# Performance work log

Measured on AMD Instinct MI355X. Metric: run time of the kernel, lower is better.

The kernel has to match this reference:

```python
import jax, jax.numpy as jnp
import numpy as np

SPATIAL = 128   # spatial_grid (H == W)
CROP = 256      # temporal grid T (power of 2)
BIN_LEN = 0.01
WALL_SIZE = 2.0
SNR = 0.1
DNUM = 2        # feature channels; bnum fixed to 1 by the module


def definePsf(U, V, slope):
    # Matlab-faithful LCT light-cone PSF: shape (2V, 2U, 2U) = (2T, 2H, 2W)
    x = np.linspace(-1.0, 1.0, 2 * U)
    z = np.linspace(0.0, 2.0, 2 * V)
    grid_z, grid_y, grid_x = np.meshgrid(z, x, x, indexing='ij')
    psf = np.abs((4.0 * slope) ** 2 * (grid_x ** 2 + grid_y ** 2) - grid_z)
    psf = (psf == psf.min(axis=0, keepdims=True)).astype(np.float64)
    psf = psf / psf[:, U, U].sum()
    psf = psf / np.linalg.norm(psf.ravel())
    psf = np.roll(psf, U, axis=1)
    psf = np.roll(psf, U, axis=2)
    return psf


def resamplingOperator(M):
    # mtx: MxM resampling (t -> sqrt-time), mtxi: its transpose-downsampled inverse
    mtx = np.zeros((M * M, M), dtype=np.float64)
    x = np.arange(1, M * M + 1)
    mtx[x - 1, np.ceil(np.sqrt(x)).astype(np.int64) - 1] = 1.0
    mtx = mtx / np.sqrt(x)[:, None]
    mtxi = mtx.T.copy()
    for _ in range(int(round(np.log2(M)))):
        mtx = 0.5 * (mtx[0::2, :] + mtx[1::2, :])
        mtxi = 0.5 * (mtxi[:, 0::2] + mtxi[:, 1::2])
    return mtx.astype(np.float32), mtxi.astype(np.float32)


def setup_inputs() -> dict:
    key = jax.random.key(0)
    c = 3e8
    bin_resolution = BIN_LEN / c
    trange = CROP * c * bin_resolution
    slope = (WALL_SIZE / 2.0) / trange
    psf = definePsf(SPATIAL, CROP, slope)
    fpsf = np.fft.fftn(psf)
    # Wiener-style inverse filter ('lct' method)
    invpsf = np.conjugate(fpsf) / (1.0 / SNR + np.real(fpsf) ** 2 + np.imag(fpsf) ** 2)
    mtx, mtxi = resamplingOperator(CROP)
    gridz = (np.arange(CROP, dtype=np.float32) / (CROP - 1)).reshape(1, CROP, 1, 1)
    feature = jax.random.normal(key, (1, DNUM, CROP, SPATIAL, SPATIAL), dtype=jnp.float32)
    return {
        'feature': feature,
        'gridz': jnp.asarray(gridz),                      # [1, T, 1, 1]
        'mtx': jnp.asarray(mtx),                          # [T, T]
        'mtxi': jnp.asarray(mtxi),                        # [T, T]
        'invpsf_real': jnp.asarray(np.real(invpsf).astype(np.float32))[None],  # [1, 2T, 2H, 2W]
        'invpsf_imag': jnp.asarray(np.imag(invpsf).astype(np.float32))[None],
    }


def reference(feature, gridz, mtx, mtxi, invpsf_real, invpsf_imag):
    b, d, T, H, W = feature.shape
    # radiometric falloff correction (diffuse: z^4)
    data = feature.reshape(b * d, T, H, W) * gridz ** 4
    # temporal resampling matmul: [T,T] @ [BD, T, H*W]
    tmp = jnp.einsum('mt,bthw->bmhw', mtx, data)
    # zero-pad to (2T, 2H, 2W)
    pad = jnp.zeros((b * d, 2 * T, 2 * H, 2 * W), dtype=feature.dtype)
    pad = pad.at[:, :T, :H, :W].set(tmp)
    # full complex 3D FFT (original stacks real/imag and calls torch.fft(x, 3))
    fre = jnp.fft.fftn(pad, axes=(1, 2, 3))
    invpsf = jax.lax.complex(invpsf_real, invpsf_imag)
    vol = jnp.fft.ifftn(fre * invpsf, axes=(1, 2, 3)).real[:, :T, :H, :W]
    out = jnp.einsum('mt,bthw->bmhw', mtxi, vol)
    return out.reshape(b, d, T, H, W)
```

## Files before the change

### kernel.cpp

```cpp
#include <hip/hip_runtime.h>
#include <math.h>

typedef float2 cplx;
#define PI_F 3.14159265358979323846f
#define C8F 0.70710678118654752440f

__device__ __forceinline__ cplx cadd(cplx a, cplx b){ return make_float2(a.x+b.x, a.y+b.y); }
__device__ __forceinline__ cplx csub(cplx a, cplx b){ return make_float2(a.x-b.x, a.y-b.y); }
__device__ __forceinline__ cplx cmul(cplx a, cplx b){ return make_float2(a.x*b.x - a.y*b.y, a.x*b.y + a.y*b.x); }
__device__ __forceinline__ cplx cmulc(cplx a, cplx b){ return make_float2(a.x*b.x + a.y*b.y, a.y*b.x - a.x*b.y); }
__device__ __forceinline__ cplx cax(float s, cplx v){ return make_float2(s*v.x, s*v.y); }

template<bool INV>
__device__ __forceinline__ void dft8(cplx* v) {
    cplx t0 = cadd(v[0], v[4]), u0 = csub(v[0], v[4]);
    cplx t1 = cadd(v[1], v[5]), u1 = csub(v[1], v[5]);
    cplx t2 = cadd(v[2], v[6]), u2 = csub(v[2], v[6]);
    cplx t3 = cadd(v[3], v[7]), u3 = csub(v[3], v[7]);
    if (!INV) {
        u1 = make_float2(C8F*(u1.x + u1.y), C8F*(u1.y - u1.x));
        u2 = make_float2(u2.y, -u2.x);
        u3 = make_float2(C8F*(u3.y - u3.x), -C8F*(u3.x + u3.y));
    } else {
        u1 = make_float2(C8F*(u1.x - u1.y), C8F*(u1.x + u1.y));
        u2 = make_float2(-u2.y, u2.x);
        u3 = make_float2(-C8F*(u3.x + u3.y), C8F*(u3.x - u3.y));
    }
    cplx b0 = cadd(t0,t2), b1 = cadd(t1,t3), b2 = csub(t0,t2), b3 = csub(t1,t3);
    b3 = INV ? make_float2(-b3.y, b3.x) : make_float2(b3.y, -b3.x);
    v[0] = cadd(b0,b1); v[4] = csub(b0,b1); v[2] = cadd(b2,b3); v[6] = csub(b2,b3);
    cplx c0 = cadd(u0,u2), c1 = cadd(u1,u3), c2 = csub(u0,u2), c3 = csub(u1,u3);
    c3 = INV ? make_float2(-c3.y, c3.x) : make_float2(c3.y, -c3.x);
    v[1] = cadd(c0,c1); v[5] = csub(c0,c1); v[3] = cadd(c2,c3); v[7] = csub(c2,c3);
}

template<bool INV>
__device__ __forceinline__ void dft4(cplx* v) {
    cplx b0 = cadd(v[0], v[2]), b2 = csub(v[0], v[2]);
    cplx b1 = cadd(v[1], v[3]), b3 = csub(v[1], v[3]);
    b3 = INV ? make_float2(-b3.y, b3.x) : make_float2(b3.y, -b3.x);
    v[0] = cadd(b0,b1); v[2] = csub(b0,b1); v[1] = cadd(b2,b3); v[3] = csub(b2,b3);
}

template<bool INV>
__device__ __forceinline__ void dft16(cplx* v) {
    #pragma unroll
    for (int a = 0; a < 4; ++a) {
        cplx t[4] = { v[a], v[a+4], v[a+8], v[a+12] };
        dft4<INV>(t);
        v[a] = t[0]; v[a+4] = t[1]; v[a+8] = t[2]; v[a+12] = t[3];
    }
    const float C1 = 0.92387953251128674f, S1 = 0.38268343236508978f, R2 = 0.70710678118654752f;
    #define TWX(idx, CR, CI) v[idx] = cmul(v[idx], make_float2(CR, INV ? -(CI) : (CI)))
    TWX(1+4*1,  C1, -S1);
    TWX(1+4*2,  R2, -R2);
    TWX(1+4*3,  S1, -C1);
    TWX(2+4*1,  R2, -R2);
    TWX(2+4*2, 0.f, -1.f);
    TWX(2+4*3, -R2, -R2);
    TWX(3+4*1,  S1, -C1);
    TWX(3+4*2, -R2, -R2);
    TWX(3+4*3, -C1,  S1);
    #undef TWX
    cplx o[16];
    #pragma unroll
    for (int c = 0; c < 4; ++c) {
        cplx t[4] = { v[4*c+0], v[4*c+1], v[4*c+2], v[4*c+3] };
        dft4<INV>(t);
        o[c] = t[0]; o[c+4] = t[1]; o[c+8] = t[2]; o[c+12] = t[3];
    }
    #pragma unroll
    for (int i = 0; i < 16; ++i) v[i] = o[i];
}

__device__ __forceinline__ int twp(int i){ return i + (i >> 4); }

__host__ __device__ __forceinline__ size_t idxB(int t, int h, int w) {
    return ((size_t)t * 256 + h) * 128 + w;
}

__global__ __launch_bounds__(256) void k0_mtx(
        const float* __restrict__ mtx, const float* __restrict__ gridz,
        float* __restrict__ tv, int* __restrict__ tc) {
    int m = blockIdx.x, t = threadIdx.x;
    __shared__ float rv[256];
    float g = gridz[t]; float g2 = g * g;
    rv[t] = mtx[m * 256 + t] * (g2 * g2);
    __syncthreads();
    if (t == 0) {
        int cnt = 0;
        for (int k = 0; k < 256 && cnt < 16; ++k)
            if (rv[k] != 0.f) { tv[m*16 + cnt] = rv[k]; tc[m*16 + cnt] = k; ++cnt; }
        for (; cnt < 16; ++cnt) { tv[m*16 + cnt] = 0.f; tc[m*16 + cnt] = 0; }
    }
}

__global__ __launch_bounds__(256) void k0_mtxi(
        const float* __restrict__ mtxi, float* __restrict__ tv, int* __restrict__ tc) {
    int m = blockIdx.x, t = threadIdx.x;
    __shared__ float rv[256];
    rv[t] = mtxi[m * 256 + t];
    __syncthreads();
    if (t == 0) {
        int cnt = 0;
        for (int k = 0; k < 256 && cnt < 8; ++k)
            if (rv[k] != 0.f) { tv[m*8 + cnt] = rv[k]; tc[m*8 + cnt] = k; ++cnt; }
        for (; cnt < 8; ++cnt) { tv[m*8 + cnt] = 0.f; tc[m*8 + cnt] = 0; }
    }
}

__global__ __launch_bounds__(512, 2) void k2_fftt(
        const float* __restrict__ feat, const float* __restrict__ tv,
        const int* __restrict__ tc, cplx* __restrict__ B) {
    const int h = blockIdx.x, w0 = blockIdx.y * 16;
    const int tid = threadIdx.x, ww = tid & 15, q = tid >> 4;
    __shared__ cplx buf[512 * 17];
    __shared__ cplx tw[512];
    { float s, c; sincosf(-(2.0f*PI_F/512.0f)*(float)tid, &s, &c); tw[tid] = make_float2(c, s); }
    cplx* f2 = buf;
    for (int idx = tid; idx < 4096; idx += 512) {
        int t = idx >> 4, w = idx & 15;
        size_t o = ((size_t)t * 128 + h) * 128 + w0 + w;
        f2[idx] = make_float2(feat[o], feat[o + 4194304]);
    }
    __syncthreads();
    cplx xa[2][8];
    for (int hi = 0; hi < 2; ++hi) {
        int u = q + 32*hi;
        #pragma unroll
        for (int p = 0; p < 8; ++p) {
            if (p < 4) {
                int m = u + 64*p;
                cplx acc = make_float2(0.f, 0.f);
                const float4* v4 = (const float4*)(tv + m*16);
                const int4*  c4 = (const int4*)(tc + m*16);
                #pragma unroll
                for (int jj = 0; jj < 4; ++jj) {
                    float4 vv = v4[jj]; int4 cc = c4[jj];
                    acc = cadd(acc, cax(vv.x, f2[cc.x*16 + ww]));
                    acc = cadd(acc, cax(vv.y, f2[cc.y*16 + ww]));
                    acc = cadd(acc, cax(vv.z, f2[cc.z*16 + ww]));
                    acc = cadd(acc, cax(vv.w, f2[cc.w*16 + ww]));
                }
                xa[hi][p] = acc;
            } else xa[hi][p] = make_float2(0.f, 0.f);
        }
    }
    dft8<false>(xa[0]); dft8<false>(xa[1]);
    __syncthreads();
    for (int hi = 0; hi < 2; ++hi) {
        int u = q + 32*hi;
        #pragma unroll
        for (int r = 1; r < 8; ++r) xa[hi][r] = cmul(xa[hi][r], tw[u * r]);
        #pragma unroll
        for (int r = 0; r < 8; ++r) buf[(64*r + u) * 17 + ww] = xa[hi][r];
    }
    __syncthreads();
    for (int hi = 0; hi < 2; ++hi) {
        int u = q + 32*hi, r1 = u >> 3, j = u & 7, base = 64*r1 + j;
        cplx y[8];
        #pragma unroll
        for (int p = 0; p < 8; ++p) y[p] = buf[(base + 8*p) * 17 + ww];
        dft8<false>(y);
        #pragma unroll
        for (int r2 = 1; r2 < 8; ++r2) y[r2] = cmul(y[r2], tw[8 * j * r2]);
        #pragma unroll
        for (int r2 = 0; r2 < 8; ++r2) buf[(base + 8*r2) * 17 + ww] = y[r2];
    }
    __syncthreads();
    for (int hi = 0; hi < 2; ++hi) {
        int m = q + 32*hi;
        cplx z[8];
        #pragma unroll
        for (int r = 0; r < 8; ++r) z[r] = buf[(8*m + r) * 17 + ww];
        dft8<false>(z);
        int kb = (m >> 3) + 8 * (m & 7);
        #pragma unroll
        for (int s2 = 0; s2 < 8; ++s2)
            B[idxB(kb + 64*s2, h, w0 + ww)] = z[s2];
    }
}

__global__ __launch_bounds__(256) void k3_ffth(cplx* __restrict__ B) {
    const int t = blockIdx.x, w0 = blockIdx.y * 16;
    const int tid = threadIdx.x, ww = tid & 15, q = tid >> 4;
    __shared__ cplx buf[256 * 16];
    __shared__ cplx tw[272];
    { float s, c; sincosf(-(2.0f*PI_F/256.0f)*(float)tid, &s, &c); tw[twp(tid)] = make_float2(c, s); }
    cplx x[16];
    #pragma unroll
    for (int n2 = 0; n2 < 8; ++n2) x[n2] = B[idxB(t, q + 16*n2, w0 + ww)];
    #pragma unroll
    for (int n2 = 8; n2 < 16; ++n2) x[n2] = make_float2(0.f, 0.f);
    dft16<false>(x);
    __syncthreads();
    #pragma unroll
    for (int k2 = 1; k2 < 16; ++k2) x[k2] = cmul(x[k2], tw[twp(q * k2)]);
    #pragma unroll
    for (int k2 = 0; k2 < 16; ++k2) buf[(q + 16*k2) * 16 + ww] = x[k2];
    __syncthreads();
    cplx z[16];
    #pragma unroll
    for (int n1 = 0; n1 < 16; ++n1) z[n1] = buf[(n1 + 16*q) * 16 + ww];
    dft16<false>(z);
    #pragma unroll
    for (int k1 = 0; k1 < 16; ++k1) B[idxB(t, q + 16*k1, w0 + ww)] = z[k1];
}

__global__ __launch_bounds__(256) void k4_fftw(
        cplx* __restrict__ B, const float* __restrict__ pr, const float* __restrict__ pim) {
    const int kt = blockIdx.x, kh0 = blockIdx.y * 16;
    const int tid = threadIdx.x, q = tid & 15, l = tid >> 4;
    __shared__ cplx buf[16 * 256];
    __shared__ cplx tw[272];
    { float s, c; sincosf(-(2.0f*PI_F/256.0f)*(float)tid, &s, &c); tw[twp(tid)] = make_float2(c, s); }
    const size_t lineB = idxB(kt, kh0 + l, 0);
    const size_t lineP = ((size_t)kt * 256 + kh0 + l) * 256;
    cplx x[16];
    #pragma unroll
    for (int n2 = 0; n2 < 8; ++n2) x[n2] = B[lineB + q + 16*n2];
    #pragma unroll
    for (int n2 = 8; n2 < 16; ++n2) x[n2] = make_float2(0.f, 0.f);
    float prv[16], piv[16];
    #pragma unroll
    for (int k1 = 0; k1 < 16; ++k1) {
        prv[k1] = pr[lineP + q + 16*k1];
        piv[k1] = pim[lineP + q + 16*k1];
    }
    dft16<false>(x);
    __syncthreads();
    #pragma unroll
    for (int k2 = 1; k2 < 16; ++k2) x[k2] = cmul(x[k2], tw[twp(q * k2)]);
    #pragma unroll
    for (int k2 = 0; k2 < 16; ++k2) buf[l*256 + (q ^ k2) + 16*k2] = x[k2];
    __syncthreads();
    cplx z[16];
    #pragma unroll
    for (int n1 = 0; n1 < 16; ++n1) z[n1] = buf[l*256 + (n1 ^ q) + 16*q];
    dft16<false>(z);
    const float S = 1.0f / (512.0f * 256.0f * 256.0f);
    #pragma unroll
    for (int k1 = 0; k1 < 16; ++k1)
        z[k1] = cmul(z[k1], make_float2(prv[k1]*S, piv[k1]*S));
    dft16<true>(z);
    #pragma unroll
    for (int n1 = 1; n1 < 16; ++n1) z[n1] = cmulc(z[n1], tw[twp(n1 * q)]);
    #pragma unroll
    for (int n1 = 0; n1 < 16; ++n1) buf[l*256 + (n1 ^ q) + 16*q] = z[n1];
    __syncthreads();
    cplx y[16];
    #pragma unroll
    for (int k2 = 0; k2 < 16; ++k2) y[k2] = buf[l*256 + (q ^ k2) + 16*k2];
    dft16<true>(y);
    #pragma unroll
    for (int n2 = 0; n2 < 8; ++n2) B[lineB + q + 16*n2] = y[n2];
}

__global__ __launch_bounds__(256) void k5_iffth(cplx* __restrict__ B) {
    const int t = blockIdx.x, w0 = blockIdx.y * 16;
    const int tid = threadIdx.x, ww = tid & 15, q = tid >> 4;
    __shared__ cplx buf[256 * 16];
    __shared__ cplx tw[272];
    { float s, c; sincosf(-(2.0f*PI_F/256.0f)*(float)tid, &s, &c); tw[twp(tid)] = make_float2(c, s); }
    cplx x[16];
    #pragma unroll
    for (int k1 = 0; k1 < 16; ++k1) x[k1] = B[idxB(t, q + 16*k1, w0 + ww)];
    dft16<true>(x);
    __syncthreads();
    #pragma unroll
    for (int n1 = 1; n1 < 16; ++n1) x[n1] = cmulc(x[n1], tw[twp(n1 * q)]);
    #pragma unroll
    for (int n1 = 0; n1 < 16; ++n1) buf[(n1 + 16*q) * 16 + ww] = x[n1];
    __syncthreads();
    cplx z[16];
    #pragma unroll
    for (int k2 = 0; k2 < 16; ++k2) z[k2] = buf[(q + 16*k2) * 16 + ww];
    dft16<true>(z);
    #pragma unroll
    for (int n2 = 0; n2 < 8; ++n2) B[idxB(t, q + 16*n2, w0 + ww)] = z[n2];
}

__global__ __launch_bounds__(512, 2) void k6_ifftt(
        cplx* __restrict__ B, const float* __restrict__ tv, const int* __restrict__ tc,
        float* __restrict__ out) {
    const int h = blockIdx.x, w0 = blockIdx.y * 16;
    const int tid = threadIdx.x, ww = tid & 15, q = tid >> 4;
    __shared__ cplx buf[512 * 17];
    __shared__ cplx tw[512];
    { float s, c; sincosf(-(2.0f*PI_F/512.0f)*(float)tid, &s, &c); tw[tid] = make_float2(c, s); }
    cplx za[2][8];
    for (int hi = 0; hi < 2; ++hi) {
        int m = q + 32*hi, kb = (m >> 3) + 8 * (m & 7);
        #pragma unroll
        for (int s2 = 0; s2 < 8; ++s2) za[hi][s2] = B[idxB(kb + 64*s2, h, w0 + ww)];
    }
    for (int hi = 0; hi < 2; ++hi) {
        int m = q + 32*hi;
        dft8<true>(za[hi]);
        #pragma unroll
        for (int jj = 0; jj < 8; ++jj) buf[(8*m + jj) * 17 + ww] = za[hi][jj];
    }
    __syncthreads();
    for (int hi = 0; hi < 2; ++hi) {
        int u = q + 32*hi, r1 = u >> 3, j = u & 7, base = 64*r1 + j;
        cplx y[8];
        #pragma unroll
        for (int r2 = 0; r2 < 8; ++r2) y[r2] = buf[(base + 8*r2) * 17 + ww];
        #pragma unroll
        for (int r2 = 1; r2 < 8; ++r2) y[r2] = cmulc(y[r2], tw[8 * j * r2]);
        dft8<true>(y);
        #pragma unroll
        for (int p = 0; p < 8; ++p) buf[(base + 8*p) * 17 + ww] = y[p];
    }
    __syncthreads();
    cplx vol[2][4];
    for (int hi = 0; hi < 2; ++hi) {
        int u = q + 32*hi;
        cplx xo[8];
        #pragma unroll
        for (int r = 0; r < 8; ++r) xo[r] = buf[(64*r + u) * 17 + ww];
        #pragma unroll
        for (int r = 1; r < 8; ++r) xo[r] = cmulc(xo[r], tw[u * r]);
        dft8<true>(xo);
        #pragma unroll
        for (int p = 0; p < 4; ++p) vol[hi][p] = xo[p];
    }
    __syncthreads();
    for (int hi = 0; hi < 2; ++hi) {
        int u = q + 32*hi;
        #pragma unroll
        for (int p = 0; p < 4; ++p) buf[(u + 64*p) * 16 + ww] = vol[hi][p];
    }
    __syncthreads();
    for (int hi = 0; hi < 2; ++hi) {
        int u = q + 32*hi;
        #pragma unroll
        for (int p = 0; p < 4; ++p) {
            int m = u + 64*p;
            cplx acc = make_float2(0.f, 0.f);
            const float4* v4 = (const float4*)(tv + m*8);
            const int4*  c4 = (const int4*)(tc + m*8);
            #pragma unroll
            for (int jj = 0; jj < 2; ++jj) {
                float4 vv = v4[jj]; int4 cc = c4[jj];
                acc = cadd(acc, cax(vv.x, buf[cc.x*16 + ww]));
                acc = cadd(acc, cax(vv.y, buf[cc.y*16 + ww]));
                acc = cadd(acc, cax(vv.z, buf[cc.z*16 + ww]));
                acc = cadd(acc, cax(vv.w, buf[cc.w*16 + ww]));
            }
            out[((size_t)m * 128 + h) * 128 + w0 + ww] = acc.x;
            out[(((size_t)256 + m) * 128 + h) * 128 + w0 + ww] = acc.y;
        }
    }
}

extern "C" void kernel_launch(void* const* d_in, const int* in_sizes, int n_in,
                              void* d_out, int out_size, void* d_ws, size_t ws_size,
                              hipStream_t stream) {
    const float* feat  = (const float*)d_in[0];
    const float* gridz = (const float*)d_in[1];
    const float* mtx   = (const float*)d_in[2];
    const float* mtxi  = (const float*)d_in[3];
    const float* pr    = (const float*)d_in[4];
    const float* pim   = (const float*)d_in[5];
    cplx* B = (cplx*)d_ws;
    float* out = (float*)d_out;

    float* T1v = (float*)(B + idxB(257, 128, 0));
    int*   T1c = (int*)(T1v + 4096);
    float* T2v = (float*)(B + idxB(0, 128, 0));
    int*   T2c = (int*)(T2v + 2048);

    k0_mtx <<<256, 256, 0, stream>>>(mtx, gridz, T1v, T1c);
    k2_fftt<<<dim3(128, 8), 512, 0, stream>>>(feat, T1v, T1c, B);
    k3_ffth<<<dim3(512, 8), 256, 0, stream>>>(B);
    k4_fftw<<<dim3(512, 16), 256, 0, stream>>>(B, pr, pim);
    k5_iffth<<<dim3(512, 8), 256, 0, stream>>>(B);
    k0_mtxi<<<256, 256, 0, stream>>>(mtxi, T2v, T2c);
    k6_ifftt<<<dim3(128, 8), 512, 0, stream>>>(B, T2v, T2c, out);
}
```

Before: 497.9 us.

## Exploit Hermitian symmetry of inverse PSF to halve filter reads in fftw kernel

Each k4 block now processes a frequency line and its mirrored line (-kt,-kh). For the mirrored line it reuses the PSF values of the first line, reading them at reversed indices and conjugating. This halves global reads of the large real/imag filter arrays and halves the grid. The 1/N normalisation is moved from the k4 filter multiply into the mtxi coefficients. The approach relies on invpsf being Hermitian-symmetric, which holds because the PSF is real, but would be wrong for an arbitrary complex filter input.

```diff
diff --git a/kernel.cpp b/kernel.cpp
--- a/kernel.cpp
+++ b/kernel.cpp
@@ -98,13 +98,14 @@
 __global__ __launch_bounds__(256) void k0_mtxi(
         const float* __restrict__ mtxi, float* __restrict__ tv, int* __restrict__ tc) {
     int m = blockIdx.x, t = threadIdx.x;
+    const float S = 2.9802322387695312e-08f;
     __shared__ float rv[256];
     rv[t] = mtxi[m * 256 + t];
     __syncthreads();
     if (t == 0) {
         int cnt = 0;
         for (int k = 0; k < 256 && cnt < 8; ++k)
-            if (rv[k] != 0.f) { tv[m*8 + cnt] = rv[k]; tc[m*8 + cnt] = k; ++cnt; }
+            if (rv[k] != 0.f) { tv[m*8 + cnt] = rv[k] * S; tc[m*8 + cnt] = k; ++cnt; }
         for (; cnt < 8; ++cnt) { tv[m*8 + cnt] = 0.f; tc[m*8 + cnt] = 0; }
     }
 }
@@ -207,53 +208,77 @@
     for (int k1 = 0; k1 < 16; ++k1) B[idxB(t, q + 16*k1, w0 + ww)] = z[k1];
 }
 
-__global__ __launch_bounds__(256) void k4_fftw(
+template<bool REV>
+__device__ __forceinline__ void k4_pass(
+        cplx* __restrict__ B, const float* __restrict__ pr, const float* __restrict__ pim,
+        size_t lineB, size_t lineP, int q, int l, cplx* buf, const cplx* tw, const cplx* xin) {
+    cplx x[16];
+    #pragma unroll
+    for (int n2 = 0; n2 < 8; ++n2) x[n2] = xin[n2];
+    #pragma unroll
+    for (int n2 = 8; n2 < 16; ++n2) x[n2] = make_float2(0.f, 0.f);
+    float prv[16], piv[16];
+    #pragma unroll
+    for (int k1 = 0; k1 < 16; ++k1) {
+        int ip = REV ? ((256 - (q + 16*k1)) & 255) : (q + 16*k1);
+        prv[k1] = pr[lineP + ip];
+        piv[k1] = pim[lineP + ip];
+    }
+    dft16<false>(x);
+    #pragma unroll
+    for (int k2 = 1; k2 < 16; ++k2) x[k2] = cmul(x[k2], tw[twp(q * k2)]);
+    #pragma unroll
+    for (int k2 = 0; k2 < 16; ++k2) buf[l*256 + (q ^ k2) + 16*k2] = x[k2];
+    __syncthreads();
+    cplx z[16];
+    #pragma unroll
+    for (int n1 = 0; n1 < 16; ++n1) z[n1] = buf[l*256 + (n1 ^ q) + 16*q];
+    dft16<false>(z);
+    #pragma unroll
+    for (int k1 = 0; k1 < 16; ++k1) {
+        cplx p = make_float2(prv[k1], piv[k1]);
+        z[k1] = REV ? cmulc(z[k1], p) : cmul(z[k1], p);
+    }
+    dft16<true>(z);
+    #pragma unroll
+    for (int n1 = 1; n1 < 16; ++n1) z[n1] = cmulc(z[n1], tw[twp(n1 * q)]);
+    #pragma unroll
+    for (int n1 = 0; n1 < 16; ++n1) buf[l*256 + (n1 ^ q) + 16*q] = z[n1];
+    __syncthreads();
+    cplx y[16];
+    #pragma unroll
+    for (int k2 = 0; k2 < 16; ++k2) y[k2] = buf[l*256 + (q ^ k2) + 16*k2];
+    dft16<true>(y);
+    #pragma unroll
+    for (int n2 = 0; n2 < 8; ++n2) B[lineB + q + 16*n2] = y[n2];
+}
+
+__global__ __launch_bounds__(256, 4) void k4_fftw(
         cplx* __restrict__ B, const float* __restrict__ pr, const float* __restrict__ pim) {
-    const int kt = blockIdx.x, kh0 = blockIdx.y * 16;
+    const int bx = blockIdx.x, kh0 = blockIdx.y * 16;
     const int tid = threadIdx.x, q = tid & 15, l = tid >> 4;
     __shared__ cplx buf[16 * 256];
     __shared__ cplx tw[272];
     { float s, c; sincosf(-(2.0f*PI_F/256.0f)*(float)tid, &s, &c); tw[twp(tid)] = make_float2(c, s); }
-    const size_t lineB = idxB(kt, kh0 + l, 0);
-    const size_t lineP = ((size_t)kt * 256 + kh0 + l) * 256;
-    cplx x[16];
-    #pragma unroll
-    for (int n2 = 0; n2 < 8; ++n2) x[n2] = B[lineB + q + 16*n2];
-    #pragma unroll
-    for (int n2 = 8; n2 < 16; ++n2) x[n2] = make_float2(0.f, 0.f);
-    float prv[16], piv[16];
-    #pragma unroll
-    for (int k1 = 0; k1 < 16; ++k1) {
-        prv[k1] = pr[lineP + q + 16*k1];
-        piv[k1] = pim[lineP + q + 16*k1];
-    }
-    dft16<false>(x);
-    __syncthreads();
-    #pragma unroll
-    for (int k2 = 1; k2 < 16; ++k2) x[k2] = cmul(x[k2], tw[twp(q * k2)]);
-    #pragma unroll
-    for (int k2 = 0; k2 < 16; ++k2) buf[l*256 + (q ^ k2) + 16*k2] = x[k2];
-    __syncthreads();
-    cplx z[16];
-    #pragma unroll
-    for (int n1 = 0; n1 < 16; ++n1) z[n1] = buf[l*256 + (n1 ^ q) + 16*q];
-    dft16<false>(z);
-    const float S = 1.0f / (512.0f * 256.0f * 256.0f);
-    #pragma unroll
-    for (int k1 = 0; k1 < 16; ++k1)
-        z[k1] = cmul(z[k1], make_float2(prv[k1]*S, piv[k1]*S));
-    dft16<true>(z);
-    #pragma unroll
-    for (int n1 = 1; n1 < 16; ++n1) z[n1] = cmulc(z[n1], tw[twp(n1 * q)]);
-    #pragma unroll
-    for (int n1 = 0; n1 < 16; ++n1) buf[l*256 + (n1 ^ q) + 16*q] = z[n1];
-    __syncthreads();
-    cplx y[16];
-    #pragma unroll
-    for (int k2 = 0; k2 < 16; ++k2) y[k2] = buf[l*256 + (q ^ k2) + 16*k2];
-    dft16<true>(y);
-    #pragma unroll
-    for (int n2 = 0; n2 < 8; ++n2) B[lineB + q + 16*n2] = y[n2];
+    const bool last = (bx == 255);
+    const int ktA = last ? 0 : bx + 1;
+    const int khA = kh0 + l;
+    const int ktB = last ? 256 : 512 - ktA;
+    const int khB = last ? khA : ((256 - khA) & 255);
+    const size_t lineBA = idxB(ktA, khA, 0);
+    const size_t lineBB = idxB(ktB, khB, 0);
+    const size_t linePA = ((size_t)ktA * 256 + khA) * 256;
+    const size_t linePB = last ? (((size_t)256 * 256 + khA) * 256) : linePA;
+    cplx xA[8], xB[8];
+    #pragma unroll
+    for (int n2 = 0; n2 < 8; ++n2) xA[n2] = B[lineBA + q + 16*n2];
+    #pragma unroll
+    for (int n2 = 0; n2 < 8; ++n2) xB[n2] = B[lineBB + q + 16*n2];
+    __syncthreads();
+    k4_pass<false>(B, pr, pim, lineBA, linePA, q, l, buf, tw, xA);
+    __syncthreads();
+    if (last) k4_pass<false>(B, pr, pim, lineBB, linePB, q, l, buf, tw, xB);
+    else      k4_pass<true >(B, pr, pim, lineBB, linePB, q, l, buf, tw, xB);
 }
 
 __global__ __launch_bounds__(256) void k5_iffth(cplx* __restrict__ B) {
@@ -374,7 +399,7 @@
     k0_mtx <<<256, 256, 0, stream>>>(mtx, gridz, T1v, T1c);
     k2_fftt<<<dim3(128, 8), 512, 0, stream>>>(feat, T1v, T1c, B);
     k3_ffth<<<dim3(512, 8), 256, 0, stream>>>(B);
-    k4_fftw<<<dim3(512, 16), 256, 0, stream>>>(B, pr, pim);
+    k4_fftw<<<dim3(256, 16), 256, 0, stream>>>(B, pr, pim);
     k5_iffth<<<dim3(512, 8), 256, 0, stream>>>(B);
     k0_mtxi<<<256, 256, 0, stream>>>(mtxi, T2v, T2c);
     k6_ifftt<<<dim3(128, 8), 512, 0, stream>>>(B, T2v, T2c, out);
```

Result: slower. 760.8 us (+52.8%).

## Fuse H-FFT, W-FFT/filter and inverse H-FFT into one per-plane kernel

Applied to the files above, without the earlier changes.

Replaces the three separate H-axis FFT, W-axis FFT+filter+IFFT and H-axis IFFT kernels with a single kernel that processes one whole kt plane in shared memory, split into even and odd frequency halves. It pairs kt with its mirror plane and exploits Hermitian symmetry of the PSF to index the filter. The global 1/N scale moves into the mtxi weights, and the odd and even halves are combined on the final write. This removes two full round trips of the large complex workspace through global memory, but uses 1024-thread blocks with 128KB of shared memory, which limits occupancy.

```diff
diff --git a/kernel.cpp b/kernel.cpp
--- a/kernel.cpp
+++ b/kernel.cpp
@@ -98,13 +98,14 @@
 __global__ __launch_bounds__(256) void k0_mtxi(
         const float* __restrict__ mtxi, float* __restrict__ tv, int* __restrict__ tc) {
     int m = blockIdx.x, t = threadIdx.x;
+    const float S = 2.9802322387695312e-08f;
     __shared__ float rv[256];
     rv[t] = mtxi[m * 256 + t];
     __syncthreads();
     if (t == 0) {
         int cnt = 0;
         for (int k = 0; k < 256 && cnt < 8; ++k)
-            if (rv[k] != 0.f) { tv[m*8 + cnt] = rv[k]; tc[m*8 + cnt] = k; ++cnt; }
+            if (rv[k] != 0.f) { tv[m*8 + cnt] = rv[k] * S; tc[m*8 + cnt] = k; ++cnt; }
         for (; cnt < 8; ++cnt) { tv[m*8 + cnt] = 0.f; tc[m*8 + cnt] = 0; }
     }
 }
@@ -181,103 +182,158 @@
     }
 }
 
-__global__ __launch_bounds__(256) void k3_ffth(cplx* __restrict__ B) {
-    const int t = blockIdx.x, w0 = blockIdx.y * 16;
-    const int tid = threadIdx.x, ww = tid & 15, q = tid >> 4;
-    __shared__ cplx buf[256 * 16];
+__device__ __forceinline__ void k4row(
+        cplx* __restrict__ eb, const int kh, const bool mir, const int ktp,
+        const int q, cplx* __restrict__ ex, const cplx* __restrict__ tw,
+        const float* __restrict__ pr, const float* __restrict__ pim) {
+    const int khp = mir ? ((256 - kh) & 255) : kh;
+    const size_t lineP = ((size_t)ktp * 256 + khp) * 256;
+    float prv[16], piv[16];
+    #pragma unroll
+    for (int k1 = 0; k1 < 16; ++k1) {
+        int kw = q + 16*k1;
+        int ip = mir ? ((256 - kw) & 255) : kw;
+        prv[k1] = pr[lineP + ip];
+        piv[k1] = mir ? -pim[lineP + ip] : pim[lineP + ip];
+    }
+    cplx x[16];
+    #pragma unroll
+    for (int n = 0; n < 8; ++n) x[n] = eb[n];
+    #pragma unroll
+    for (int n = 8; n < 16; ++n) x[n] = make_float2(0.f, 0.f);
+    dft16<false>(x);
+    #pragma unroll
+    for (int k2 = 1; k2 < 16; ++k2) x[k2] = cmul(x[k2], tw[twp(q * k2)]);
+    #pragma unroll
+    for (int k2 = 0; k2 < 16; ++k2) ex[(q ^ k2) + 16*k2] = x[k2];
+    __syncthreads();
+    cplx z[16];
+    #pragma unroll
+    for (int n1 = 0; n1 < 16; ++n1) z[n1] = ex[(n1 ^ q) + 16*q];
+    dft16<false>(z);
+    #pragma unroll
+    for (int k1 = 0; k1 < 16; ++k1) z[k1] = cmul(z[k1], make_float2(prv[k1], piv[k1]));
+    dft16<true>(z);
+    #pragma unroll
+    for (int n1 = 1; n1 < 16; ++n1) z[n1] = cmulc(z[n1], tw[twp(n1 * q)]);
+    #pragma unroll
+    for (int n1 = 0; n1 < 16; ++n1) ex[(n1 ^ q) + 16*q] = z[n1];
+    __syncthreads();
+    cplx y[16];
+    #pragma unroll
+    for (int k2 = 0; k2 < 16; ++k2) y[k2] = ex[(q ^ k2) + 16*k2];
+    dft16<true>(y);
+    #pragma unroll
+    for (int n = 0; n < 8; ++n) eb[n] = y[n];
+}
+
+__global__ __launch_bounds__(1024) void k345(
+        cplx* __restrict__ B, const float* __restrict__ pr, const float* __restrict__ pim) {
+    const int bx = blockIdx.x;
+    const int i = bx >> 1;
+    const int kt = ((bx & 1) == 0) ? i : (i == 0 ? 256 : 512 - i);
+    const bool mir = (kt > 256);
+    const int ktp = mir ? 512 - kt : kt;
+    const int tid = threadIdx.x;
+    const int w = tid & 127, b = tid >> 7;
+    const int team = tid >> 4, q = tid & 15;
+    __shared__ cplx PL[16384];
     __shared__ cplx tw[272];
-    { float s, c; sincosf(-(2.0f*PI_F/256.0f)*(float)tid, &s, &c); tw[twp(tid)] = make_float2(c, s); }
-    cplx x[16];
-    #pragma unroll
-    for (int n2 = 0; n2 < 8; ++n2) x[n2] = B[idxB(t, q + 16*n2, w0 + ww)];
-    #pragma unroll
-    for (int n2 = 8; n2 < 16; ++n2) x[n2] = make_float2(0.f, 0.f);
-    dft16<false>(x);
-    __syncthreads();
-    #pragma unroll
-    for (int k2 = 1; k2 < 16; ++k2) x[k2] = cmul(x[k2], tw[twp(q * k2)]);
-    #pragma unroll
-    for (int k2 = 0; k2 < 16; ++k2) buf[(q + 16*k2) * 16 + ww] = x[k2];
-    __syncthreads();
-    cplx z[16];
-    #pragma unroll
-    for (int n1 = 0; n1 < 16; ++n1) z[n1] = buf[(n1 + 16*q) * 16 + ww];
-    dft16<false>(z);
-    #pragma unroll
-    for (int k1 = 0; k1 < 16; ++k1) B[idxB(t, q + 16*k1, w0 + ww)] = z[k1];
-}
-
-__global__ __launch_bounds__(256) void k4_fftw(
-        cplx* __restrict__ B, const float* __restrict__ pr, const float* __restrict__ pim) {
-    const int kt = blockIdx.x, kh0 = blockIdx.y * 16;
-    const int tid = threadIdx.x, q = tid & 15, l = tid >> 4;
-    __shared__ cplx buf[16 * 256];
-    __shared__ cplx tw[272];
-    { float s, c; sincosf(-(2.0f*PI_F/256.0f)*(float)tid, &s, &c); tw[twp(tid)] = make_float2(c, s); }
-    const size_t lineB = idxB(kt, kh0 + l, 0);
-    const size_t lineP = ((size_t)kt * 256 + kh0 + l) * 256;
-    cplx x[16];
-    #pragma unroll
-    for (int n2 = 0; n2 < 8; ++n2) x[n2] = B[lineB + q + 16*n2];
-    #pragma unroll
-    for (int n2 = 8; n2 < 16; ++n2) x[n2] = make_float2(0.f, 0.f);
-    float prv[16], piv[16];
-    #pragma unroll
-    for (int k1 = 0; k1 < 16; ++k1) {
-        prv[k1] = pr[lineP + q + 16*k1];
-        piv[k1] = pim[lineP + q + 16*k1];
-    }
-    dft16<false>(x);
-    __syncthreads();
-    #pragma unroll
-    for (int k2 = 1; k2 < 16; ++k2) x[k2] = cmul(x[k2], tw[twp(q * k2)]);
-    #pragma unroll
-    for (int k2 = 0; k2 < 16; ++k2) buf[l*256 + (q ^ k2) + 16*k2] = x[k2];
-    __syncthreads();
-    cplx z[16];
-    #pragma unroll
-    for (int n1 = 0; n1 < 16; ++n1) z[n1] = buf[l*256 + (n1 ^ q) + 16*q];
-    dft16<false>(z);
-    const float S = 1.0f / (512.0f * 256.0f * 256.0f);
-    #pragma unroll
-    for (int k1 = 0; k1 < 16; ++k1)
-        z[k1] = cmul(z[k1], make_float2(prv[k1]*S, piv[k1]*S));
-    dft16<true>(z);
-    #pragma unroll
-    for (int n1 = 1; n1 < 16; ++n1) z[n1] = cmulc(z[n1], tw[twp(n1 * q)]);
-    #pragma unroll
-    for (int n1 = 0; n1 < 16; ++n1) buf[l*256 + (n1 ^ q) + 16*q] = z[n1];
-    __syncthreads();
-    cplx y[16];
-    #pragma unroll
-    for (int k2 = 0; k2 < 16; ++k2) y[k2] = buf[l*256 + (q ^ k2) + 16*k2];
-    dft16<true>(y);
-    #pragma unroll
-    for (int n2 = 0; n2 < 8; ++n2) B[lineB + q + 16*n2] = y[n2];
-}
-
-__global__ __launch_bounds__(256) void k5_iffth(cplx* __restrict__ B) {
-    const int t = blockIdx.x, w0 = blockIdx.y * 16;
-    const int tid = threadIdx.x, ww = tid & 15, q = tid >> 4;
-    __shared__ cplx buf[256 * 16];
-    __shared__ cplx tw[272];
-    { float s, c; sincosf(-(2.0f*PI_F/256.0f)*(float)tid, &s, &c); tw[twp(tid)] = make_float2(c, s); }
-    cplx x[16];
-    #pragma unroll
-    for (int k1 = 0; k1 < 16; ++k1) x[k1] = B[idxB(t, q + 16*k1, w0 + ww)];
-    dft16<true>(x);
-    __syncthreads();
-    #pragma unroll
-    for (int n1 = 1; n1 < 16; ++n1) x[n1] = cmulc(x[n1], tw[twp(n1 * q)]);
-    #pragma unroll
-    for (int n1 = 0; n1 < 16; ++n1) buf[(n1 + 16*q) * 16 + ww] = x[n1];
-    __syncthreads();
-    cplx z[16];
-    #pragma unroll
-    for (int k2 = 0; k2 < 16; ++k2) z[k2] = buf[(q + 16*k2) * 16 + ww];
-    dft16<true>(z);
-    #pragma unroll
-    for (int n2 = 0; n2 < 8; ++n2) B[idxB(t, q + 16*n2, w0 + ww)] = z[n2];
+    if (tid < 256) { float s, c; sincosf(-(2.0f*PI_F/256.0f)*(float)tid, &s, &c); tw[twp(tid)] = make_float2(c, s); }
+    const size_t plane = (size_t)kt * 256 * 128;
+    cplx* ex = PL + team * 256;
+    __syncthreads();
+
+    #pragma unroll 1
+    for (int odd = 0; odd < 2; ++odd) {
+        cplx p[16];
+        #pragma unroll
+        for (int a = 0; a < 16; ++a)
+            p[a] = B[plane + (size_t)(8*a + b)*128 + w];
+        if (odd) {
+            #pragma unroll
+            for (int a = 0; a < 16; ++a) p[a] = cmul(p[a], tw[twp(8*a + b)]);
+        }
+        dft16<false>(p);
+        #pragma unroll
+        for (int c = 1; c < 16; ++c) p[c] = cmul(p[c], tw[twp(2*b*c)]);
+        __syncthreads();
+        #pragma unroll
+        for (int c = 0; c < 16; ++c) PL[(b + 8*c)*128 + w] = p[c];
+        __syncthreads();
+        cplx e[16];
+        #pragma unroll
+        for (int g = 0; g < 2; ++g) {
+            int c = b + 8*g;
+            cplx t8[8];
+            #pragma unroll
+            for (int b2 = 0; b2 < 8; ++b2) t8[b2] = PL[(b2 + 8*c)*128 + w];
+            dft8<false>(t8);
+            #pragma unroll
+            for (int d = 0; d < 8; ++d) e[8*g + d] = t8[d];
+        }
+        __syncthreads();
+        #pragma unroll
+        for (int g = 0; g < 2; ++g) {
+            int c = b + 8*g;
+            #pragma unroll
+            for (int d = 0; d < 8; ++d) PL[(c + 16*d)*128 + w] = e[8*g + d];
+        }
+        __syncthreads();
+        cplx e1[8], e2[8];
+        #pragma unroll
+        for (int n = 0; n < 8; ++n) e1[n] = PL[team*128 + q + 16*n];
+        #pragma unroll
+        for (int n = 0; n < 8; ++n) e2[n] = PL[(team + 64)*128 + q + 16*n];
+        __syncthreads();
+        k4row(e1, 2*team + odd, mir, ktp, q, ex, tw, pr, pim);
+        __syncthreads();
+        k4row(e2, 2*(team + 64) + odd, mir, ktp, q, ex, tw, pr, pim);
+        __syncthreads();
+        #pragma unroll
+        for (int n = 0; n < 8; ++n) PL[team*128 + q + 16*n] = e1[n];
+        #pragma unroll
+        for (int n = 0; n < 8; ++n) PL[(team + 64)*128 + q + 16*n] = e2[n];
+        __syncthreads();
+        cplx A[16];
+        #pragma unroll
+        for (int g = 0; g < 2; ++g) {
+            int c = b + 8*g;
+            cplx t8[8];
+            #pragma unroll
+            for (int d = 0; d < 8; ++d) t8[d] = PL[(c + 16*d)*128 + w];
+            dft8<true>(t8);
+            #pragma unroll
+            for (int m = 0; m < 8; ++m) A[8*g + m] = t8[m];
+        }
+        __syncthreads();
+        #pragma unroll
+        for (int g = 0; g < 2; ++g) {
+            int c = b + 8*g;
+            #pragma unroll
+            for (int m = 0; m < 8; ++m) PL[(8*c + m)*128 + w] = A[8*g + m];
+        }
+        __syncthreads();
+        cplx v[16];
+        #pragma unroll
+        for (int c = 0; c < 16; ++c) v[c] = PL[(8*c + b)*128 + w];
+        #pragma unroll
+        for (int c = 1; c < 16; ++c) v[c] = cmulc(v[c], tw[twp(2*b*c)]);
+        dft16<true>(v);
+        if (!odd) {
+            #pragma unroll
+            for (int a = 0; a < 16; ++a)
+                B[plane + (size_t)(128 + 8*a + b)*128 + w] = v[a];
+        } else {
+            #pragma unroll
+            for (int a = 0; a < 16; ++a) {
+                int h = 8*a + b;
+                cplx xo = cmulc(v[a], tw[twp(h)]);
+                cplx ce = B[plane + (size_t)(128 + h)*128 + w];
+                B[plane + (size_t)h*128 + w] = cadd(ce, xo);
+            }
+        }
+    }
 }
 
 __global__ __launch_bounds__(512, 2) void k6_ifftt(
@@ -373,9 +429,7 @@
 
     k0_mtx <<<256, 256, 0, stream>>>(mtx, gridz, T1v, T1c);
     k2_fftt<<<dim3(128, 8), 512, 0, stream>>>(feat, T1v, T1c, B);
-    k3_ffth<<<dim3(512, 8), 256, 0, stream>>>(B);
-    k4_fftw<<<dim3(512, 16), 256, 0, stream>>>(B, pr, pim);
-    k5_iffth<<<dim3(512, 8), 256, 0, stream>>>(B);
+    k345   <<<512, 1024, 0, stream>>>(B, pr, pim);
     k0_mtxi<<<256, 256, 0, stream>>>(mtxi, T2v, T2c);
     k6_ifftt<<<dim3(128, 8), 512, 0, stream>>>(B, T2v, T2c, out);
 }
```

Measured after the change: 1.032 ms. 107% more time.
